# Optimization experiments

Hardware: AMD Instinct MI355X
Metric: run time of the kernel (lower is better)

The kernel has to match this reference:

```python
import jax, jax.numpy as jnp
import numpy as np

B, C_IN, C_MID, C_OUT, R, K = 2048, 64, 64, 128, 60, 13
EPS = 1e-5


def _gather(x, nei):
    # x: [B, C, 60] -> gather neighbors -> [B, C, 60, 13]
    b, c = x.shape[0], x.shape[1]
    return x[:, :, nei].reshape(b, c, R, K)


def _block(x, nei, g, bta, m, v, W, c):
    # BN (eval mode) -> ReLU -> Conv2d(kernel (1,13)) fused block.
    h = _gather(x, nei)                              # [B,C,60,13]
    inv = g * jax.lax.rsqrt(v + EPS)                 # [C]
    h = jax.nn.relu(h * inv[None, :, None, None] + (bta - m * inv)[None, :, None, None])
    # Conv2d with kernel (1,13), stride 1 == contraction over (c, k)
    return jnp.einsum('bcrk,ock->bor', h, W) + c[None, :, None]  # [B,O,60]


def setup_inputs() -> dict:
    key = jax.random.key(0)
    ks = jax.random.split(key, 24)
    n = lambda k, s: jax.random.normal(k, s, dtype=jnp.float32)
    u = lambda k, s: jax.random.uniform(k, s, dtype=jnp.float32, minval=0.5, maxval=1.5)
    return {
        "x": n(ks[0], (B, C_IN, R)),
        "nei": jax.random.randint(ks[1], (R * K,), 0, R, dtype=jnp.int32),
        # comb_layer_in: BN(in) + Conv(in->mid)
        "g1": n(ks[2], (C_IN,)), "b1": n(ks[3], (C_IN,)), "m1": n(ks[4], (C_IN,)), "v1": u(ks[5], (C_IN,)),
        "W1": n(ks[6], (C_MID, C_IN, K)) * 0.1, "c1": n(ks[7], (C_MID,)) * 0.1,
        # comb_layer_out: BN(mid) + Conv(mid->out)
        "g2": n(ks[8], (C_MID,)), "b2": n(ks[9], (C_MID,)), "m2": n(ks[10], (C_MID,)), "v2": u(ks[11], (C_MID,)),
        "W2": n(ks[12], (C_OUT, C_MID, K)) * 0.1, "c2": n(ks[13], (C_OUT,)) * 0.1,
        # short_cut_layer: BN(in) + Conv(in->out)
        "g3": n(ks[14], (C_IN,)), "b3": n(ks[15], (C_IN,)), "m3": n(ks[16], (C_IN,)), "v3": u(ks[17], (C_IN,)),
        "W3": n(ks[18], (C_OUT, C_IN, K)) * 0.1, "c3": n(ks[19], (C_OUT,)) * 0.1,
    }


def reference(x, nei, g1, b1, m1, v1, W1, c1, g2, b2, m2, v2, W2, c2,
              g3, b3, m3, v3, W3, c3):
    f = _block(x, nei, g1, b1, m1, v1, W1, c1)      # [B, C_MID, 60]
    f = _block(f, nei, g2, b2, m2, v2, W2, c2)      # [B, C_OUT, 60]
    sc = _block(x, nei, g3, b3, m3, v3, W3, c3)     # [B, C_OUT, 60]
    return f + sc
```

## Files before the change

### kernel.cpp

```cpp
#include <hip/hip_runtime.h>
#include <hip/hip_bf16.h>


typedef __attribute__((ext_vector_type(8))) short bf16x8;
typedef __attribute__((ext_vector_type(4))) float f32x4;
typedef __attribute__((ext_vector_type(4))) unsigned short us4;
typedef __attribute__((ext_vector_type(8))) unsigned short us8;

#define EPSV 1e-5f
#define PLANE 131072
#define ZTOT  7864320
#define LDSTR 72

__device__ __forceinline__ unsigned short f2bf(float f) {
  unsigned int u = __builtin_bit_cast(unsigned int, f);
  u += 0x7FFFu + ((u >> 16) & 1u);
  return (unsigned short)(u >> 16);
}
__device__ __forceinline__ float bf2f(unsigned short s) {
  unsigned int u = ((unsigned int)s) << 16;
  return __builtin_bit_cast(float, u);
}

__global__ void prep_p(const float* __restrict__ g1, const float* __restrict__ be1,
                       const float* __restrict__ mu1, const float* __restrict__ va1,
                       const float* __restrict__ c1,
                       const float* __restrict__ g2, const float* __restrict__ be2,
                       const float* __restrict__ mu2, const float* __restrict__ va2,
                       const float* __restrict__ c2,
                       const float* __restrict__ g3, const float* __restrict__ be3,
                       const float* __restrict__ mu3, const float* __restrict__ va3,
                       const float* __restrict__ c3,
                       float* __restrict__ params) {
  int t = threadIdx.x;
  if (t < 64) {
    float a1v = g1[t] * rsqrtf(va1[t] + EPSV);
    params[t]       = a1v;
    params[64 + t]  = be1[t] - mu1[t] * a1v;
    float a3v = g3[t] * rsqrtf(va3[t] + EPSV);
    params[128 + t] = a3v;
    params[192 + t] = be3[t] - mu3[t] * a3v;
    float a2v = g2[t] * rsqrtf(va2[t] + EPSV);
    params[256 + t] = a2v;
    params[320 + t] = be2[t] - mu2[t] * a2v + a2v * c1[t];
  }
  if (t < 128) params[384 + t] = c2[t] + c3[t];
}

__global__ void prep_w(const float* __restrict__ W1, const float* __restrict__ W2,
                       const float* __restrict__ W3, unsigned short* __restrict__ W1t,
                       unsigned short* __restrict__ W23t) {
  int t = blockIdx.x * 256 + threadIdx.x;
  if (t < 4096) {
    int o = t >> 6, c = t & 63;
    const float* src = W1 + (o * 64 + c) * 13;
    unsigned short* dst = W1t + o * 832 + c;
    #pragma unroll
    for (int ks = 0; ks < 13; ks++) dst[ks * 64] = f2bf(src[ks]);
  } else if (t < 20480) {
    int idx = t - 4096;
    int half = idx >> 13;
    int o = (idx >> 6) & 127, c = idx & 63;
    const float* src = (half ? W3 : W2) + (o * 64 + c) * 13;
    unsigned short* dst = W23t + o * 1664 + half * 13 * 64 + c;
    #pragma unroll
    for (int ks = 0; ks < 13; ks++) dst[ks * 64] = f2bf(src[ks]);
  }
}

__global__ __launch_bounds__(256) void t_in(const float* __restrict__ x,
                                            const float* __restrict__ params,
                                            unsigned short* __restrict__ z1T,
                                            unsigned short* __restrict__ z3T) {
  __shared__ float xt[64 * 61];
  __shared__ float prm[256];
  const int b = blockIdx.x, t = threadIdx.x;
  prm[t] = params[t];
  for (int i = t; i < 3840; i += 256) {
    int c = i / 60;
    xt[c * 61 + (i - c * 60)] = x[b * 3840 + i];
  }
  __syncthreads();
  if (t < 240) {
    int r = t >> 2, g = t & 3, c0 = g << 4;
    us8 z1v0, z1v1, z3v0, z3v1;
    #pragma unroll
    for (int j = 0; j < 8; j++) {
      int c = c0 + j;
      float v = xt[c * 61 + r];
      z1v0[j] = f2bf(fmaxf(fmaf(v, prm[c], prm[64 + c]), 0.f));
      z3v0[j] = f2bf(fmaxf(fmaf(v, prm[128 + c], prm[192 + c]), 0.f));
    }
    #pragma unroll
    for (int j = 0; j < 8; j++) {
      int c = c0 + 8 + j;
      float v = xt[c * 61 + r];
      z1v1[j] = f2bf(fmaxf(fmaf(v, prm[c], prm[64 + c]), 0.f));
      z3v1[j] = f2bf(fmaxf(fmaf(v, prm[128 + c], prm[192 + c]), 0.f));
    }
    int idx = (r * 2048 + b) * 64 + c0;
    *(us8*)(z1T + idx) = z1v0;  *(us8*)(z1T + idx + 8) = z1v1;
    *(us8*)(z3T + idx) = z3v0;  *(us8*)(z3T + idx + 8) = z3v1;
  }
}

#define MFMA __builtin_amdgcn_mfma_f32_16x16x32_bf16

__global__ __launch_bounds__(256, 2) void gemm1(const unsigned short* __restrict__ W1t,
                                                const unsigned short* __restrict__ z1T,
                                                const int* __restrict__ nei,
                                                const float* __restrict__ params,
                                                unsigned short* __restrict__ z2T) {
  __shared__ unsigned short As[2][64 * LDSTR];
  __shared__ unsigned short Bs[2][128 * LDSTR];

  const int bid = blockIdx.x;
  const int btile = bid / 60, r = bid - btile * 60;
  const int b0 = btile << 7;
  const int t = threadIdx.x, wave = t >> 6, lane = t & 63;
  const int quad = lane >> 4, nl = lane & 15;
  const int mh = wave >> 1, nh = wave & 1;

  int pl[13];
  #pragma unroll
  for (int q = 0; q < 13; q++) pl[q] = nei[r * 13 + q];

  const int trow = t >> 3, tj = t & 7;
  const unsigned short* gA = W1t + trow * 832 + tj * 8;
  const unsigned short* gB = z1T + (b0 + trow) * 64 + tj * 8;
  unsigned short* lA = &As[0][0] + trow * LDSTR + tj * 8;
  unsigned short* lB = &Bs[0][0] + trow * LDSTR + tj * 8;

  {
    us8 va0 = *(const us8*)(gA);
    us8 va1 = *(const us8*)(gA + 32 * 832);
    const unsigned short* gb = gB + pl[0] * PLANE;
    us8 vb0 = *(const us8*)(gb);
    us8 vb1 = *(const us8*)(gb + 2048);
    us8 vb2 = *(const us8*)(gb + 4096);
    us8 vb3 = *(const us8*)(gb + 6144);
    *(us8*)(lA) = va0;
    *(us8*)(lA + 32 * LDSTR) = va1;
    *(us8*)(lB) = vb0;
    *(us8*)(lB + 32 * LDSTR) = vb1;
    *(us8*)(lB + 64 * LDSTR) = vb2;
    *(us8*)(lB + 96 * LDSTR) = vb3;
  }
  __syncthreads();

  f32x4 acc[2][4] = {};
  #pragma unroll 1
  for (int kq = 0; kq < 13; kq++) {
    const int bf = kq & 1;
    us8 va0, va1, vb0, vb1, vb2, vb3;
    if (kq < 12) {
      const unsigned short* ga = gA + (kq + 1) * 64;
      va0 = *(const us8*)(ga);
      va1 = *(const us8*)(ga + 32 * 832);
      const unsigned short* gb = gB + pl[kq + 1] * PLANE;
      vb0 = *(const us8*)(gb);
      vb1 = *(const us8*)(gb + 2048);
      vb2 = *(const us8*)(gb + 4096);
      vb3 = *(const us8*)(gb + 6144);
    }
    const unsigned short* Ab = &As[bf][0] + (mh * 32 + nl) * LDSTR + quad * 8;
    const unsigned short* Bb = &Bs[bf][0] + (nh * 64 + nl) * LDSTR + quad * 8;
    bf16x8 af[2][2], bfr[4][2];
    #pragma unroll
    for (int mt = 0; mt < 2; mt++) {
      af[mt][0] = *(const bf16x8*)(Ab + mt * 16 * LDSTR);
      af[mt][1] = *(const bf16x8*)(Ab + mt * 16 * LDSTR + 32);
    }
    #pragma unroll
    for (int nt = 0; nt < 4; nt++) {
      bfr[nt][0] = *(const bf16x8*)(Bb + nt * 16 * LDSTR);
      bfr[nt][1] = *(const bf16x8*)(Bb + nt * 16 * LDSTR + 32);
    }
    #pragma unroll
    for (int h = 0; h < 2; h++) {
      #pragma unroll
      for (int mt = 0; mt < 2; mt++) {
        #pragma unroll
        for (int nt = 0; nt < 4; nt++) {
          acc[mt][nt] = MFMA(af[mt][h], bfr[nt][h], acc[mt][nt], 0, 0, 0);
        }
      }
    }
    if (kq < 12) {
      unsigned short* la = lA + (bf ^ 1) * (64 * LDSTR);
      unsigned short* lb = lB + (bf ^ 1) * (128 * LDSTR);
      *(us8*)(la) = va0;
      *(us8*)(la + 32 * LDSTR) = va1;
      *(us8*)(lb) = vb0;
      *(us8*)(lb + 32 * LDSTR) = vb1;
      *(us8*)(lb + 64 * LDSTR) = vb2;
      *(us8*)(lb + 96 * LDSTR) = vb3;
    }
    __syncthreads();
  }

  #pragma unroll
  for (int mt = 0; mt < 2; mt++) {
    int ob = mh * 32 + mt * 16 + quad * 4;
    f32x4 av = *(const f32x4*)(params + 256 + ob);
    f32x4 bv = *(const f32x4*)(params + 320 + ob);
    #pragma unroll
    for (int nt = 0; nt < 4; nt++) {
      int col = b0 + nh * 64 + nt * 16 + nl;
      f32x4 a = acc[mt][nt];
      us4 w;
      w.x = f2bf(fmaxf(fmaf(a[0], av[0], bv[0]), 0.f));
      w.y = f2bf(fmaxf(fmaf(a[1], av[1], bv[1]), 0.f));
      w.z = f2bf(fmaxf(fmaf(a[2], av[2], bv[2]), 0.f));
      w.w = f2bf(fmaxf(fmaf(a[3], av[3], bv[3]), 0.f));
      *(us4*)(z2T + (r * 2048 + col) * 64 + ob) = w;
    }
  }
}

__global__ __launch_bounds__(256, 2) void gemm2(const unsigned short* __restrict__ W23t,
                                                const unsigned short* __restrict__ z2T,
                                                const unsigned short* __restrict__ z3T,
                                                const int* __restrict__ nei,
                                                const float* __restrict__ params,
                                                unsigned short* __restrict__ outT) {
  __shared__ unsigned short As[2][128 * LDSTR];
  __shared__ unsigned short Bs[2][128 * LDSTR];

  const int bid = blockIdx.x;
  const int btile = bid / 60, r = bid - btile * 60;
  const int b0 = btile << 7;
  const int t = threadIdx.x, wave = t >> 6, lane = t & 63;
  const int quad = lane >> 4, nl = lane & 15;
  const int mh = wave >> 1, nh = wave & 1;

  int pl[13];
  #pragma unroll
  for (int q = 0; q < 13; q++) pl[q] = nei[r * 13 + q];

  const int trow = t >> 3, tj = t & 7;
  const unsigned short* gA  = W23t + trow * 1664 + tj * 8;
  const unsigned short* gB2 = z2T + (b0 + trow) * 64 + tj * 8;
  const unsigned short* gB3 = z3T + (b0 + trow) * 64 + tj * 8;
  unsigned short* lA = &As[0][0] + trow * LDSTR + tj * 8;
  unsigned short* lB = &Bs[0][0] + trow * LDSTR + tj * 8;

  {
    us8 va0 = *(const us8*)(gA);
    us8 va1 = *(const us8*)(gA + 32 * 1664);
    us8 va2 = *(const us8*)(gA + 64 * 1664);
    us8 va3 = *(const us8*)(gA + 96 * 1664);
    const unsigned short* gb = gB2 + pl[0] * PLANE;
    us8 vb0 = *(const us8*)(gb);
    us8 vb1 = *(const us8*)(gb + 2048);
    us8 vb2 = *(const us8*)(gb + 4096);
    us8 vb3 = *(const us8*)(gb + 6144);
    *(us8*)(lA) = va0;
    *(us8*)(lA + 32 * LDSTR) = va1;
    *(us8*)(lA + 64 * LDSTR) = va2;
    *(us8*)(lA + 96 * LDSTR) = va3;
    *(us8*)(lB) = vb0;
    *(us8*)(lB + 32 * LDSTR) = vb1;
    *(us8*)(lB + 64 * LDSTR) = vb2;
    *(us8*)(lB + 96 * LDSTR) = vb3;
  }
  __syncthreads();

  f32x4 acc[4][4] = {};
  #pragma unroll 1
  for (int kq = 0; kq < 26; kq++) {
    const int bf = kq & 1;
    us8 va0, va1, va2, va3, vb0, vb1, vb2, vb3;
    if (kq < 25) {
      const int kn = kq + 1;
      const unsigned short* ga = gA + kn * 64;
      va0 = *(const us8*)(ga);
      va1 = *(const us8*)(ga + 32 * 1664);
      va2 = *(const us8*)(ga + 64 * 1664);
      va3 = *(const us8*)(ga + 96 * 1664);
      const unsigned short* gb = (kn < 13) ? (gB2 + pl[kn] * PLANE)
                                           : (gB3 + pl[kn - 13] * PLANE);
      vb0 = *(const us8*)(gb);
      vb1 = *(const us8*)(gb + 2048);
      vb2 = *(const us8*)(gb + 4096);
      vb3 = *(const us8*)(gb + 6144);
    }
    const unsigned short* Ab = &As[bf][0] + (mh * 64 + nl) * LDSTR + quad * 8;
    const unsigned short* Bb = &Bs[bf][0] + (nh * 64 + nl) * LDSTR + quad * 8;
    bf16x8 af[4][2], bfr[4][2];
    #pragma unroll
    for (int mt = 0; mt < 4; mt++) {
      af[mt][0] = *(const bf16x8*)(Ab + mt * 16 * LDSTR);
      af[mt][1] = *(const bf16x8*)(Ab + mt * 16 * LDSTR + 32);
    }
    #pragma unroll
    for (int nt = 0; nt < 4; nt++) {
      bfr[nt][0] = *(const bf16x8*)(Bb + nt * 16 * LDSTR);
      bfr[nt][1] = *(const bf16x8*)(Bb + nt * 16 * LDSTR + 32);
    }
    #pragma unroll
    for (int h = 0; h < 2; h++) {
      #pragma unroll
      for (int mt = 0; mt < 4; mt++) {
        #pragma unroll
        for (int nt = 0; nt < 4; nt++) {
          acc[mt][nt] = MFMA(af[mt][h], bfr[nt][h], acc[mt][nt], 0, 0, 0);
        }
      }
    }
    if (kq < 25) {
      unsigned short* la = lA + (bf ^ 1) * (128 * LDSTR);
      unsigned short* lb = lB + (bf ^ 1) * (128 * LDSTR);
      *(us8*)(la) = va0;
      *(us8*)(la + 32 * LDSTR) = va1;
      *(us8*)(la + 64 * LDSTR) = va2;
      *(us8*)(la + 96 * LDSTR) = va3;
      *(us8*)(lb) = vb0;
      *(us8*)(lb + 32 * LDSTR) = vb1;
      *(us8*)(lb + 64 * LDSTR) = vb2;
      *(us8*)(lb + 96 * LDSTR) = vb3;
    }
    __syncthreads();
  }

  #pragma unroll
  for (int mt = 0; mt < 4; mt++) {
    int ob = mh * 64 + mt * 16 + quad * 4;
    f32x4 cv = *(const f32x4*)(params + 384 + ob);
    #pragma unroll
    for (int nt = 0; nt < 4; nt++) {
      int col = b0 + nh * 64 + nt * 16 + nl;
      f32x4 a = acc[mt][nt];
      us4 w;
      w.x = f2bf(a[0] + cv[0]);
      w.y = f2bf(a[1] + cv[1]);
      w.z = f2bf(a[2] + cv[2]);
      w.w = f2bf(a[3] + cv[3]);
      *(us4*)(outT + (r * 2048 + col) * 128 + ob) = w;
    }
  }
}

__global__ __launch_bounds__(256) void t_out(const unsigned short* __restrict__ outT,
                                             float* __restrict__ out) {
  __shared__ float ot[60 * 129];
  const int b = blockIdx.x, t = threadIdx.x;
  for (int i = t; i < 1920; i += 256) {
    int r = i >> 5, og = (i & 31) << 2;
    us4 v = *(const us4*)(outT + (r * 2048 + b) * 128 + og);
    ot[r * 129 + og + 0] = bf2f(v.x);
    ot[r * 129 + og + 1] = bf2f(v.y);
    ot[r * 129 + og + 2] = bf2f(v.z);
    ot[r * 129 + og + 3] = bf2f(v.w);
  }
  __syncthreads();
  int o = t >> 1, s = t & 1;
  float* dst = out + b * 7680 + o * 60 + s * 30;
  #pragma unroll
  for (int j = 0; j < 30; j++) dst[j] = ot[(s * 30 + j) * 129 + o];
}

extern "C" void kernel_launch(void* const* d_in, const int* in_sizes, int n_in,
                              void* d_out, int out_size, void* d_ws, size_t ws_size,
                              hipStream_t stream) {
  const float* x   = (const float*)d_in[0];
  const int*   nei = (const int*)d_in[1];
  const float* g1  = (const float*)d_in[2];
  const float* be1 = (const float*)d_in[3];
  const float* mu1 = (const float*)d_in[4];
  const float* va1 = (const float*)d_in[5];
  const float* W1  = (const float*)d_in[6];
  const float* c1  = (const float*)d_in[7];
  const float* g2  = (const float*)d_in[8];
  const float* be2 = (const float*)d_in[9];
  const float* mu2 = (const float*)d_in[10];
  const float* va2 = (const float*)d_in[11];
  const float* W2  = (const float*)d_in[12];
  const float* c2  = (const float*)d_in[13];
  const float* g3  = (const float*)d_in[14];
  const float* be3 = (const float*)d_in[15];
  const float* mu3 = (const float*)d_in[16];
  const float* va3 = (const float*)d_in[17];
  const float* W3  = (const float*)d_in[18];
  const float* c3  = (const float*)d_in[19];

  unsigned short* W1t  = (unsigned short*)d_ws;
  unsigned short* W23t = W1t + 53248;
  float*          prm  = (float*)(W23t + 212992);
  unsigned short* z2T  = (unsigned short*)(prm + 512);
  unsigned short* z3T  = z2T + ZTOT;
  unsigned short* big  = z3T + ZTOT;
  unsigned short* z1T  = big;
  unsigned short* outT = big;

  prep_p<<<1, 128, 0, stream>>>(g1, be1, mu1, va1, c1, g2, be2, mu2, va2, c2,
                                g3, be3, mu3, va3, c3, prm);
  prep_w<<<80, 256, 0, stream>>>(W1, W2, W3, W1t, W23t);
  t_in<<<2048, 256, 0, stream>>>(x, prm, z1T, z3T);
  gemm1<<<960, 256, 0, stream>>>(W1t, z1T, nei, prm, z2T);
  gemm2<<<960, 256, 0, stream>>>(W23t, z2T, z3T, nei, prm, outT);
  t_out<<<2048, 256, 0, stream>>>(outT, (float*)d_out);
}
```

Baseline: 259.2 us.

## Process two output rows per gemm1 block, XOR-swizzle LDS, fuse prep kernels

gemm1 now computes two neighbour rows per block. Each block loads the W1 tile once and reuses it across two gathered B tiles, which halves the grid and the weight traffic. Both GEMMs replace padded LDS rows with an XOR-swizzled 64-wide layout to avoid bank conflicts without the padding. Block ordering changes so that consecutive blocks share a row, and the parameter-prep kernel is folded into the weight-prep kernel to save a launch. gemm1 uses more LDS per block (about 80KB) and more accumulators, which may reduce occupancy.

```diff
diff --git a/kernel.cpp b/kernel.cpp
--- a/kernel.cpp
+++ b/kernel.cpp
@@ -10,7 +10,6 @@
 #define EPSV 1e-5f
 #define PLANE 131072
 #define ZTOT  7864320
-#define LDSTR 72
 
 __device__ __forceinline__ unsigned short f2bf(float f) {
   unsigned int u = __builtin_bit_cast(unsigned int, f);
@@ -22,7 +21,9 @@
   return __builtin_bit_cast(float, u);
 }
 
-__global__ void prep_p(const float* __restrict__ g1, const float* __restrict__ be1,
+__global__ void prep_w(const float* __restrict__ W1, const float* __restrict__ W2,
+                       const float* __restrict__ W3,
+                       const float* __restrict__ g1, const float* __restrict__ be1,
                        const float* __restrict__ mu1, const float* __restrict__ va1,
                        const float* __restrict__ c1,
                        const float* __restrict__ g2, const float* __restrict__ be2,
@@ -31,25 +32,9 @@
                        const float* __restrict__ g3, const float* __restrict__ be3,
                        const float* __restrict__ mu3, const float* __restrict__ va3,
                        const float* __restrict__ c3,
+                       unsigned short* __restrict__ W1t,
+                       unsigned short* __restrict__ W23t,
                        float* __restrict__ params) {
-  int t = threadIdx.x;
-  if (t < 64) {
-    float a1v = g1[t] * rsqrtf(va1[t] + EPSV);
-    params[t]       = a1v;
-    params[64 + t]  = be1[t] - mu1[t] * a1v;
-    float a3v = g3[t] * rsqrtf(va3[t] + EPSV);
-    params[128 + t] = a3v;
-    params[192 + t] = be3[t] - mu3[t] * a3v;
-    float a2v = g2[t] * rsqrtf(va2[t] + EPSV);
-    params[256 + t] = a2v;
-    params[320 + t] = be2[t] - mu2[t] * a2v + a2v * c1[t];
-  }
-  if (t < 128) params[384 + t] = c2[t] + c3[t];
-}
-
-__global__ void prep_w(const float* __restrict__ W1, const float* __restrict__ W2,
-                       const float* __restrict__ W3, unsigned short* __restrict__ W1t,
-                       unsigned short* __restrict__ W23t) {
   int t = blockIdx.x * 256 + threadIdx.x;
   if (t < 4096) {
     int o = t >> 6, c = t & 63;
@@ -65,6 +50,21 @@
     unsigned short* dst = W23t + o * 1664 + half * 13 * 64 + c;
     #pragma unroll
     for (int ks = 0; ks < 13; ks++) dst[ks * 64] = f2bf(src[ks]);
+  }
+  if (blockIdx.x == 79) {
+    int u = threadIdx.x;
+    if (u < 64) {
+      float a1v = g1[u] * rsqrtf(va1[u] + EPSV);
+      params[u]       = a1v;
+      params[64 + u]  = be1[u] - mu1[u] * a1v;
+      float a3v = g3[u] * rsqrtf(va3[u] + EPSV);
+      params[128 + u] = a3v;
+      params[192 + u] = be3[u] - mu3[u] * a3v;
+      float a2v = g2[u] * rsqrtf(va2[u] + EPSV);
+      params[256 + u] = a2v;
+      params[320 + u] = be2[u] - mu2[u] * a2v + a2v * c1[u];
+    }
+    if (u < 128) params[384 + u] = c2[u] + c3[u];
   }
 }
 
@@ -111,109 +111,116 @@
                                                 const int* __restrict__ nei,
                                                 const float* __restrict__ params,
                                                 unsigned short* __restrict__ z2T) {
-  __shared__ unsigned short As[2][64 * LDSTR];
-  __shared__ unsigned short Bs[2][128 * LDSTR];
+  __shared__ unsigned short As[2][4096];
+  __shared__ unsigned short Bs[2][2][8192];
 
   const int bid = blockIdx.x;
-  const int btile = bid / 60, r = bid - btile * 60;
+  const int rp = bid >> 4, btile = bid & 15;
   const int b0 = btile << 7;
+  const int rA = rp * 2, rB = rA + 1;
   const int t = threadIdx.x, wave = t >> 6, lane = t & 63;
   const int quad = lane >> 4, nl = lane & 15;
-  const int mh = wave >> 1, nh = wave & 1;
-
-  int pl[13];
+  const int rsel = wave >> 1, nhh = wave & 1;
+
+  int pl0[13], pl1[13];
   #pragma unroll
-  for (int q = 0; q < 13; q++) pl[q] = nei[r * 13 + q];
+  for (int q = 0; q < 13; q++) { pl0[q] = nei[rA * 13 + q]; pl1[q] = nei[rB * 13 + q]; }
 
   const int trow = t >> 3, tj = t & 7;
+  const int sw8 = ((tj ^ (trow & 7)) << 3);
   const unsigned short* gA = W1t + trow * 832 + tj * 8;
   const unsigned short* gB = z1T + (b0 + trow) * 64 + tj * 8;
-  unsigned short* lA = &As[0][0] + trow * LDSTR + tj * 8;
-  unsigned short* lB = &Bs[0][0] + trow * LDSTR + tj * 8;
+  unsigned short* lA = &As[0][trow * 64 + sw8];
+  unsigned short* lB0 = &Bs[0][0][trow * 64 + sw8];
+  unsigned short* lB1 = &Bs[0][1][trow * 64 + sw8];
 
   {
     us8 va0 = *(const us8*)(gA);
     us8 va1 = *(const us8*)(gA + 32 * 832);
-    const unsigned short* gb = gB + pl[0] * PLANE;
-    us8 vb0 = *(const us8*)(gb);
-    us8 vb1 = *(const us8*)(gb + 2048);
-    us8 vb2 = *(const us8*)(gb + 4096);
-    us8 vb3 = *(const us8*)(gb + 6144);
-    *(us8*)(lA) = va0;
-    *(us8*)(lA + 32 * LDSTR) = va1;
-    *(us8*)(lB) = vb0;
-    *(us8*)(lB + 32 * LDSTR) = vb1;
-    *(us8*)(lB + 64 * LDSTR) = vb2;
-    *(us8*)(lB + 96 * LDSTR) = vb3;
+    const unsigned short* g0 = gB + pl0[0] * PLANE;
+    const unsigned short* g1p = gB + pl1[0] * PLANE;
+    us8 b00 = *(const us8*)(g0);
+    us8 b01 = *(const us8*)(g0 + 2048);
+    us8 b02 = *(const us8*)(g0 + 4096);
+    us8 b03 = *(const us8*)(g0 + 6144);
+    us8 b10 = *(const us8*)(g1p);
+    us8 b11 = *(const us8*)(g1p + 2048);
+    us8 b12 = *(const us8*)(g1p + 4096);
+    us8 b13 = *(const us8*)(g1p + 6144);
+    *(us8*)(lA) = va0;  *(us8*)(lA + 2048) = va1;
+    *(us8*)(lB0) = b00; *(us8*)(lB0 + 2048) = b01;
+    *(us8*)(lB0 + 4096) = b02; *(us8*)(lB0 + 6144) = b03;
+    *(us8*)(lB1) = b10; *(us8*)(lB1 + 2048) = b11;
+    *(us8*)(lB1 + 4096) = b12; *(us8*)(lB1 + 6144) = b13;
   }
   __syncthreads();
 
-  f32x4 acc[2][4] = {};
+  const int c0 = ((quad ^ (nl & 7)) << 3);
+  f32x4 acc[4][4] = {};
   #pragma unroll 1
   for (int kq = 0; kq < 13; kq++) {
     const int bf = kq & 1;
-    us8 va0, va1, vb0, vb1, vb2, vb3;
+    us8 va0, va1, b00, b01, b02, b03, b10, b11, b12, b13;
     if (kq < 12) {
       const unsigned short* ga = gA + (kq + 1) * 64;
       va0 = *(const us8*)(ga);
       va1 = *(const us8*)(ga + 32 * 832);
-      const unsigned short* gb = gB + pl[kq + 1] * PLANE;
-      vb0 = *(const us8*)(gb);
-      vb1 = *(const us8*)(gb + 2048);
-      vb2 = *(const us8*)(gb + 4096);
-      vb3 = *(const us8*)(gb + 6144);
-    }
-    const unsigned short* Ab = &As[bf][0] + (mh * 32 + nl) * LDSTR + quad * 8;
-    const unsigned short* Bb = &Bs[bf][0] + (nh * 64 + nl) * LDSTR + quad * 8;
-    bf16x8 af[2][2], bfr[4][2];
-    #pragma unroll
-    for (int mt = 0; mt < 2; mt++) {
-      af[mt][0] = *(const bf16x8*)(Ab + mt * 16 * LDSTR);
-      af[mt][1] = *(const bf16x8*)(Ab + mt * 16 * LDSTR + 32);
+      const unsigned short* g0 = gB + pl0[kq + 1] * PLANE;
+      const unsigned short* g1p = gB + pl1[kq + 1] * PLANE;
+      b00 = *(const us8*)(g0);        b01 = *(const us8*)(g0 + 2048);
+      b02 = *(const us8*)(g0 + 4096); b03 = *(const us8*)(g0 + 6144);
+      b10 = *(const us8*)(g1p);        b11 = *(const us8*)(g1p + 2048);
+      b12 = *(const us8*)(g1p + 4096); b13 = *(const us8*)(g1p + 6144);
+    }
+    const unsigned short* Ab = &As[bf][nl * 64];
+    const unsigned short* Bb = &Bs[bf][rsel][(nhh * 64 + nl) * 64];
+    bf16x8 af[4][2], bfr[4][2];
+    #pragma unroll
+    for (int mt = 0; mt < 4; mt++) {
+      af[mt][0] = *(const bf16x8*)(Ab + mt * 1024 + c0);
+      af[mt][1] = *(const bf16x8*)(Ab + mt * 1024 + (c0 ^ 32));
     }
     #pragma unroll
     for (int nt = 0; nt < 4; nt++) {
-      bfr[nt][0] = *(const bf16x8*)(Bb + nt * 16 * LDSTR);
-      bfr[nt][1] = *(const bf16x8*)(Bb + nt * 16 * LDSTR + 32);
-    }
-    #pragma unroll
-    for (int h = 0; h < 2; h++) {
+      bfr[nt][0] = *(const bf16x8*)(Bb + nt * 1024 + c0);
+      bfr[nt][1] = *(const bf16x8*)(Bb + nt * 1024 + (c0 ^ 32));
+    }
+    #pragma unroll
+    for (int h = 0; h < 2; h++)
       #pragma unroll
-      for (int mt = 0; mt < 2; mt++) {
+      for (int mt = 0; mt < 4; mt++)
         #pragma unroll
-        for (int nt = 0; nt < 4; nt++) {
+        for (int nt = 0; nt < 4; nt++)
           acc[mt][nt] = MFMA(af[mt][h], bfr[nt][h], acc[mt][nt], 0, 0, 0);
-        }
-      }
-    }
     if (kq < 12) {
-      unsigned short* la = lA + (bf ^ 1) * (64 * LDSTR);
-      unsigned short* lb = lB + (bf ^ 1) * (128 * LDSTR);
-      *(us8*)(la) = va0;
-      *(us8*)(la + 32 * LDSTR) = va1;
-      *(us8*)(lb) = vb0;
-      *(us8*)(lb + 32 * LDSTR) = vb1;
-      *(us8*)(lb + 64 * LDSTR) = vb2;
-      *(us8*)(lb + 96 * LDSTR) = vb3;
+      unsigned short* la = lA + (bf ^ 1) * 4096;
+      unsigned short* l0 = lB0 + (bf ^ 1) * 16384;
+      unsigned short* l1 = lB1 + (bf ^ 1) * 16384;
+      *(us8*)(la) = va0;  *(us8*)(la + 2048) = va1;
+      *(us8*)(l0) = b00; *(us8*)(l0 + 2048) = b01;
+      *(us8*)(l0 + 4096) = b02; *(us8*)(l0 + 6144) = b03;
+      *(us8*)(l1) = b10; *(us8*)(l1 + 2048) = b11;
+      *(us8*)(l1 + 4096) = b12; *(us8*)(l1 + 6144) = b13;
     }
     __syncthreads();
   }
 
+  const int rr = rA + rsel;
   #pragma unroll
-  for (int mt = 0; mt < 2; mt++) {
-    int ob = mh * 32 + mt * 16 + quad * 4;
+  for (int mt = 0; mt < 4; mt++) {
+    int ob = mt * 16 + quad * 4;
     f32x4 av = *(const f32x4*)(params + 256 + ob);
     f32x4 bv = *(const f32x4*)(params + 320 + ob);
     #pragma unroll
     for (int nt = 0; nt < 4; nt++) {
-      int col = b0 + nh * 64 + nt * 16 + nl;
+      int col = b0 + nhh * 64 + nt * 16 + nl;
       f32x4 a = acc[mt][nt];
       us4 w;
       w.x = f2bf(fmaxf(fmaf(a[0], av[0], bv[0]), 0.f));
       w.y = f2bf(fmaxf(fmaf(a[1], av[1], bv[1]), 0.f));
       w.z = f2bf(fmaxf(fmaf(a[2], av[2], bv[2]), 0.f));
       w.w = f2bf(fmaxf(fmaf(a[3], av[3], bv[3]), 0.f));
-      *(us4*)(z2T + (r * 2048 + col) * 64 + ob) = w;
+      *(us4*)(z2T + (rr * 2048 + col) * 64 + ob) = w;
     }
   }
 }
@@ -224,11 +231,11 @@
                                                 const int* __restrict__ nei,
                                                 const float* __restrict__ params,
                                                 unsigned short* __restrict__ outT) {
-  __shared__ unsigned short As[2][128 * LDSTR];
-  __shared__ unsigned short Bs[2][128 * LDSTR];
+  __shared__ unsigned short As[2][8192];
+  __shared__ unsigned short Bs[2][8192];
 
   const int bid = blockIdx.x;
-  const int btile = bid / 60, r = bid - btile * 60;
+  const int r = bid >> 4, btile = bid & 15;
   const int b0 = btile << 7;
   const int t = threadIdx.x, wave = t >> 6, lane = t & 63;
   const int quad = lane >> 4, nl = lane & 15;
@@ -239,11 +246,12 @@
   for (int q = 0; q < 13; q++) pl[q] = nei[r * 13 + q];
 
   const int trow = t >> 3, tj = t & 7;
+  const int sw8 = ((tj ^ (trow & 7)) << 3);
   const unsigned short* gA  = W23t + trow * 1664 + tj * 8;
   const unsigned short* gB2 = z2T + (b0 + trow) * 64 + tj * 8;
   const unsigned short* gB3 = z3T + (b0 + trow) * 64 + tj * 8;
-  unsigned short* lA = &As[0][0] + trow * LDSTR + tj * 8;
-  unsigned short* lB = &Bs[0][0] + trow * LDSTR + tj * 8;
+  unsigned short* lA = &As[0][trow * 64 + sw8];
+  unsigned short* lB = &Bs[0][trow * 64 + sw8];
 
   {
     us8 va0 = *(const us8*)(gA);
@@ -255,17 +263,14 @@
     us8 vb1 = *(const us8*)(gb + 2048);
     us8 vb2 = *(const us8*)(gb + 4096);
     us8 vb3 = *(const us8*)(gb + 6144);
-    *(us8*)(lA) = va0;
-    *(us8*)(lA + 32 * LDSTR) = va1;
-    *(us8*)(lA + 64 * LDSTR) = va2;
-    *(us8*)(lA + 96 * LDSTR) = va3;
-    *(us8*)(lB) = vb0;
-    *(us8*)(lB + 32 * LDSTR) = vb1;
-    *(us8*)(lB + 64 * LDSTR) = vb2;
-    *(us8*)(lB + 96 * LDSTR) = vb3;
+    *(us8*)(lA) = va0;        *(us8*)(lA + 2048) = va1;
+    *(us8*)(lA + 4096) = va2; *(us8*)(lA + 6144) = va3;
+    *(us8*)(lB) = vb0;        *(us8*)(lB + 2048) = vb1;
+    *(us8*)(lB + 4096) = vb2; *(us8*)(lB + 6144) = vb3;
   }
   __syncthreads();
 
+  const int c0 = ((quad ^ (nl & 7)) << 3);
   f32x4 acc[4][4] = {};
   #pragma unroll 1
   for (int kq = 0; kq < 26; kq++) {
@@ -285,40 +290,33 @@
       vb2 = *(const us8*)(gb + 4096);
       vb3 = *(const us8*)(gb + 6144);
     }
-    const unsigned short* Ab = &As[bf][0] + (mh * 64 + nl) * LDSTR + quad * 8;
-    const unsigned short* Bb = &Bs[bf][0] + (nh * 64 + nl) * LDSTR + quad * 8;
+    const unsigned short* Ab = &As[bf][(mh * 64 + nl) * 64];
+    const unsigned short* Bb = &Bs[bf][(nh * 64 + nl) * 64];
     bf16x8 af[4][2], bfr[4][2];
     #pragma unroll
     for (int mt = 0; mt < 4; mt++) {
-      af[mt][0] = *(const bf16x8*)(Ab + mt * 16 * LDSTR);
-      af[mt][1] = *(const bf16x8*)(Ab + mt * 16 * LDSTR + 32);
+      af[mt][0] = *(const bf16x8*)(Ab + mt * 1024 + c0);
+      af[mt][1] = *(const bf16x8*)(Ab + mt * 1024 + (c0 ^ 32));
     }
     #pragma unroll
     for (int nt = 0; nt < 4; nt++) {
-      bfr[nt][0] = *(const bf16x8*)(Bb + nt * 16 * LDSTR);
-      bfr[nt][1] = *(const bf16x8*)(Bb + nt * 16 * LDSTR + 32);
-    }
-    #pragma unroll
-    for (int h = 0; h < 2; h++) {
+      bfr[nt][0] = *(const bf16x8*)(Bb + nt * 1024 + c0);
+      bfr[nt][1] = *(const bf16x8*)(Bb + nt * 1024 + (c0 ^ 32));
+    }
+    #pragma unroll
+    for (int h = 0; h < 2; h++)
       #pragma unroll
-      for (int mt = 0; mt < 4; mt++) {
+      for (int mt = 0; mt < 4; mt++)
         #pragma unroll
-        for (int nt = 0; nt < 4; nt++) {
+        for (int nt = 0; nt < 4; nt++)
           acc[mt][nt] = MFMA(af[mt][h], bfr[nt][h], acc[mt][nt], 0, 0, 0);
-        }
-      }
-    }
     if (kq < 25) {
-      unsigned short* la = lA + (bf ^ 1) * (128 * LDSTR);
-      unsigned short* lb = lB + (bf ^ 1) * (128 * LDSTR);
-      *(us8*)(la) = va0;
-      *(us8*)(la + 32 * LDSTR) = va1;
-      *(us8*)(la + 64 * LDSTR) = va2;
-      *(us8*)(la + 96 * LDSTR) = va3;
-      *(us8*)(lb) = vb0;
-      *(us8*)(lb + 32 * LDSTR) = vb1;
-      *(us8*)(lb + 64 * LDSTR) = vb2;
-      *(us8*)(lb + 96 * LDSTR) = vb3;
+      unsigned short* la = lA + (bf ^ 1) * 8192;
+      unsigned short* lb = lB + (bf ^ 1) * 8192;
+      *(us8*)(la) = va0;        *(us8*)(la + 2048) = va1;
+      *(us8*)(la + 4096) = va2; *(us8*)(la + 6144) = va3;
+      *(us8*)(lb) = vb0;        *(us8*)(lb + 2048) = vb1;
+      *(us8*)(lb + 4096) = vb2; *(us8*)(lb + 6144) = vb3;
     }
     __syncthreads();
   }
@@ -393,11 +391,13 @@
   unsigned short* z1T  = big;
   unsigned short* outT = big;
 
-  prep_p<<<1, 128, 0, stream>>>(g1, be1, mu1, va1, c1, g2, be2, mu2, va2, c2,
-                                g3, be3, mu3, va3, c3, prm);
-  prep_w<<<80, 256, 0, stream>>>(W1, W2, W3, W1t, W23t);
+  prep_w<<<80, 256, 0, stream>>>(W1, W2, W3,
+                                 g1, be1, mu1, va1, c1,
+                                 g2, be2, mu2, va2, c2,
+                                 g3, be3, mu3, va3, c3,
+                                 W1t, W23t, prm);
   t_in<<<2048, 256, 0, stream>>>(x, prm, z1T, z3T);
-  gemm1<<<960, 256, 0, stream>>>(W1t, z1T, nei, prm, z2T);
+  gemm1<<<480, 256, 0, stream>>>(W1t, z1T, nei, prm, z2T);
   gemm2<<<960, 256, 0, stream>>>(W23t, z2T, z3T, nei, prm, outT);
   t_out<<<2048, 256, 0, stream>>>(outT, (float*)d_out);
 }
```

Measured after the change: 249.6 us. 1.04x faster.
